# Optimization experiments

Measured on AMD Instinct MI355X. Metric: run time of the kernel, lower is better.

## Reference

```python
import jax, jax.numpy as jnp
import numpy as np

N_INPUT = 2
N_NODES = 4
C = 64          # channel width of every state
B, H, W = 64, 32, 32
N_EDGES = sum(N_INPUT + i for i in range(N_NODES))  # 2+3+4+5 = 14


def conv1x1(x, w):
    # x: [B,C,H,W], w: [C_out,C_in] -> [B,C_out,H,W]
    return jnp.einsum('bchw,oc->bohw', x, w)


def setup_inputs() -> dict:
    key = jax.random.key(0)
    k0, k1, k2, k3 = jax.random.split(key, 4)
    x0 = jax.random.normal(k0, (B, C, H, W), dtype=jnp.float32)
    x1 = jax.random.normal(k1, (B, C, H, W), dtype=jnp.float32)
    # preproc: one 1x1 conv per input state
    W_pre = jax.random.normal(k2, (N_INPUT, C, C), dtype=jnp.float32) * (1.0 / np.sqrt(C))
    # one 1x1 conv per DAG edge (flattened in enumeration order)
    W_edge = jax.random.normal(k3, (N_EDGES, C, C), dtype=jnp.float32) * (1.0 / np.sqrt(C))
    return {'x0': x0, 'x1': x1, 'W_pre': W_pre, 'W_edge': W_edge}


def reference(x0, x1, W_pre, W_edge):
    # preprocess inputs -> initial states
    states = [conv1x1(x0, W_pre[0]), conv1x1(x1, W_pre[1])]
    e = 0
    for i in range(N_NODES):
        n_states = N_INPUT + i
        # gather every prior state, apply edge op (ReLU -> 1x1 conv), sum-merge
        s_cur = conv1x1(jax.nn.relu(states[0]), W_edge[e])
        for s in range(1, n_states):
            s_cur = s_cur + conv1x1(jax.nn.relu(states[s]), W_edge[e + s])
        e += n_states
        states.append(s_cur)
    # merger_out: concat intermediate node states (start=n_input) on channels
    return jnp.concatenate(states[N_INPUT:], axis=1)  # [B, N_NODES*C, H, W]
```

## Files before the change

kernel.cpp:

```cpp
#include <hip/hip_runtime.h>


typedef _Float16 f16;
typedef _Float16 f16x8 __attribute__((ext_vector_type(8)));
typedef float    f32x4 __attribute__((ext_vector_type(4)));

#define RSH 72
#define SB  (64 * RSH)

__device__ __forceinline__ unsigned int pkrtz(float a, float b) {
    __fp16 h2 __attribute__((ext_vector_type(2))) = __builtin_amdgcn_cvt_pkrtz(a, b);
    return __builtin_bit_cast(unsigned int, h2);
}

__global__ __launch_bounds__(256, 2) void dag_kernel(
    const float* __restrict__ x0, const float* __restrict__ x1,
    const float* __restrict__ Wpre, const float* __restrict__ Wedge,
    float* __restrict__ out)
{
    __shared__ __align__(16) f16 lds[7 * SB];

    const int t    = threadIdx.x;
    const int lane = t & 63;
    const int w    = t >> 6;
    const int pl   = lane & 15;
    const int q    = lane >> 4;
    const int mb0  = (w & 1) * 2;
    const int nb0  = (w >> 1) * 2;

    const int blk = blockIdx.x;
    const int b   = blk >> 4;
    const int hw0 = (blk & 15) * 64;

    const float* xg[2] = { x0 + b * 65536 + hw0, x1 + b * 65536 + hw0 };
    float* outg = out + b * 262144 + hw0;

    {
        const int p  = t & 63;
        const int cg = t >> 6;
        #pragma unroll
        for (int inp = 0; inp < 2; ++inp) {
            const float* src = xg[inp] + (cg * 16) * 1024 + p;
            unsigned int u[8];
            #pragma unroll
            for (int i = 0; i < 8; ++i)
                u[i] = pkrtz(src[(2 * i) * 1024], src[(2 * i + 1) * 1024]);
            f16* dst = lds + (3 + inp) * SB + p * RSH + cg * 16;
            ((uint4*)dst)[0] = make_uint4(u[0], u[1], u[2], u[3]);
            ((uint4*)dst)[1] = make_uint4(u[4], u[5], u[6], u[7]);
        }
    }
    {
        const int o = t >> 2, cq = t & 3;
        const float4* ws = (const float4*)(Wpre + o * 64 + cq * 16);
        unsigned int u[8];
        #pragma unroll
        for (int i = 0; i < 4; ++i) {
            float4 v = ws[i];
            u[2 * i]     = pkrtz(v.x, v.y);
            u[2 * i + 1] = pkrtz(v.z, v.w);
        }
        f16* dst = lds + 5 * SB + o * RSH + cq * 16;
        ((uint4*)dst)[0] = make_uint4(u[0], u[1], u[2], u[3]);
        ((uint4*)dst)[1] = make_uint4(u[4], u[5], u[6], u[7]);
    }

    f32x4 acc[2][2] = {};

    #pragma unroll
    for (int k = 0; k < 16; ++k) {
        const int src_tab[16] = { 3,4, 0,1, 0,1,2, 0,1,2,3, 0,1,2,3,4 };
        const int dst_tab[16] = { 0,1, -1,2, -1,-1,3, -1,-1,-1,4, -1,-1,-1,-1,-1 };
        const int out_tab[16] = { -1,-1, -1,0, -1,-1,1, -1,-1,-1,2, -1,-1,-1,-1,3 };

        __syncthreads();

        float4 wr[4];
        if (k < 15) {
            const float* wsrc = ((k + 1 < 2) ? (Wpre + (k + 1) * 4096)
                                             : (Wedge + (k - 1) * 4096))
                                + (t >> 2) * 64 + (t & 3) * 16;
            #pragma unroll
            for (int i = 0; i < 4; ++i) wr[i] = ((const float4*)wsrc)[i];
        }

        const f16* Wl = lds + (5 + (k & 1)) * SB;
        const f16* S  = lds + src_tab[k] * SB;
        #pragma unroll
        for (int kb = 0; kb < 2; ++kb) {
            f16x8 af[2], bf[2];
            #pragma unroll
            for (int i = 0; i < 2; ++i)
                af[i] = *(const f16x8*)(Wl + ((mb0 + i) * 16 + pl) * RSH + kb * 32 + q * 8);
            #pragma unroll
            for (int j = 0; j < 2; ++j)
                bf[j] = *(const f16x8*)(S + ((nb0 + j) * 16 + pl) * RSH + kb * 32 + q * 8);
            #pragma unroll
            for (int i = 0; i < 2; ++i)
                #pragma unroll
                for (int j = 0; j < 2; ++j)
                    acc[i][j] = __builtin_amdgcn_mfma_f32_16x16x32_f16(
                                    af[i], bf[j], acc[i][j], 0, 0, 0);
        }

        if (out_tab[k] >= 0) {
            #pragma unroll
            for (int i = 0; i < 2; ++i)
                #pragma unroll
                for (int j = 0; j < 2; ++j) {
                    const int c = (mb0 + i) * 16 + q * 4;
                    const int p = (nb0 + j) * 16 + pl;
                    #pragma unroll
                    for (int r = 0; r < 4; ++r)
                        outg[(out_tab[k] * 64 + c + r) * 1024 + p] = acc[i][j][r];
                }
        }
        if (dst_tab[k] >= 0) {
            f16* D = lds + dst_tab[k] * SB;
            #pragma unroll
            for (int i = 0; i < 2; ++i)
                #pragma unroll
                for (int j = 0; j < 2; ++j) {
                    const int c = (mb0 + i) * 16 + q * 4;
                    const int p = (nb0 + j) * 16 + pl;
                    unsigned int u0 = pkrtz(fmaxf(acc[i][j][0], 0.f), fmaxf(acc[i][j][1], 0.f));
                    unsigned int u1 = pkrtz(fmaxf(acc[i][j][2], 0.f), fmaxf(acc[i][j][3], 0.f));
                    *(uint2*)(D + p * RSH + c) = make_uint2(u0, u1);
                }
            #pragma unroll
            for (int i = 0; i < 2; ++i)
                #pragma unroll
                for (int j = 0; j < 2; ++j)
                    acc[i][j] = (f32x4){0.f, 0.f, 0.f, 0.f};
        }

        if (k < 15) {
            unsigned int u[8];
            #pragma unroll
            for (int i = 0; i < 4; ++i) {
                u[2 * i]     = pkrtz(wr[i].x, wr[i].y);
                u[2 * i + 1] = pkrtz(wr[i].z, wr[i].w);
            }
            f16* dst = lds + (5 + ((k + 1) & 1)) * SB + (t >> 2) * RSH + (t & 3) * 16;
            ((uint4*)dst)[0] = make_uint4(u[0], u[1], u[2], u[3]);
            ((uint4*)dst)[1] = make_uint4(u[4], u[5], u[6], u[7]);
        }
    }
}

extern "C" void kernel_launch(void* const* d_in, const int* in_sizes, int n_in,
                              void* d_out, int out_size, void* d_ws, size_t ws_size,
                              hipStream_t stream) {
    const float* x0    = (const float*)d_in[0];
    const float* x1    = (const float*)d_in[1];
    const float* Wpre  = (const float*)d_in[2];
    const float* Wedge = (const float*)d_in[3];
    float* outp        = (float*)d_out;
    dag_kernel<<<dim3(1024), dim3(256), 0, stream>>>(x0, x1, Wpre, Wedge, outp);
}
```

Baseline: 114.7 us.

## Pre-convert weights to fp16 MFMA fragments, load into registers, drop per-step barriers

A small pre-kernel converts all 16 weight matrices to fp16 in the MFMA A-fragment layout, stored in the workspace. The main kernel loads each weight matrix straight from global memory into registers, double-buffered one step ahead, instead of staging it through LDS. Each wave now owns a 16-pixel column strip and covers all 64 output channels, so intermediate states are written and read only by the same wave. That removes the per-step __syncthreads, shrinks LDS from 7 to 5 buffers, and raises the occupancy hint to 3 blocks. The costs are an extra kernel launch, more register pressure from holding weight fragments, and redundant global or L2 weight reads in every block.

```diff
diff --git a/kernel.cpp b/kernel.cpp
--- a/kernel.cpp
+++ b/kernel.cpp
@@ -13,20 +13,34 @@
     return __builtin_bit_cast(unsigned int, h2);
 }
 
-__global__ __launch_bounds__(256, 2) void dag_kernel(
+__global__ __launch_bounds__(256) void wconv_kernel(
+    const float* __restrict__ Wpre, const float* __restrict__ Wedge,
+    f16* __restrict__ ws)
+{
+    const int u   = blockIdx.x * 256 + threadIdx.x;
+    const int k   = u >> 9;
+    const int rem = u & 511;
+    const int g   = rem >> 6;
+    const int row = rem & 63;
+    const float* src = ((k < 2) ? (Wpre + k * 4096) : (Wedge + (k - 2) * 4096))
+                       + row * 64 + (g >> 2) * 32 + (g & 3) * 8;
+    float4 v0 = ((const float4*)src)[0];
+    float4 v1 = ((const float4*)src)[1];
+    ((uint4*)ws)[u] = make_uint4(pkrtz(v0.x, v0.y), pkrtz(v0.z, v0.w),
+                                 pkrtz(v1.x, v1.y), pkrtz(v1.z, v1.w));
+}
+
+__global__ __launch_bounds__(256, 3) void dag_kernel(
     const float* __restrict__ x0, const float* __restrict__ x1,
-    const float* __restrict__ Wpre, const float* __restrict__ Wedge,
-    float* __restrict__ out)
+    const f16* __restrict__ wf, float* __restrict__ out)
 {
-    __shared__ __align__(16) f16 lds[7 * SB];
+    __shared__ __align__(16) f16 lds[5 * SB];
 
     const int t    = threadIdx.x;
     const int lane = t & 63;
-    const int w    = t >> 6;
+    const int wv   = t >> 6;
     const int pl   = lane & 15;
     const int q    = lane >> 4;
-    const int mb0  = (w & 1) * 2;
-    const int nb0  = (w >> 1) * 2;
 
     const int blk = blockIdx.x;
     const int b   = blk >> 4;
@@ -35,9 +49,17 @@
     const float* xg[2] = { x0 + b * 65536 + hw0, x1 + b * 65536 + hw0 };
     float* outg = out + b * 262144 + hw0;
 
+    const f16* wl = wf + q * 512 + pl * 8;
+
+    f16x8 wA[2][2][4];
+    #pragma unroll
+    for (int kb = 0; kb < 2; ++kb)
+        #pragma unroll
+        for (int i = 0; i < 4; ++i)
+            wA[0][kb][i] = *(const f16x8*)(wl + kb * 2048 + i * 128);
+
     {
-        const int p  = t & 63;
-        const int cg = t >> 6;
+        const int p = t & 63, cg = t >> 6;
         #pragma unroll
         for (int inp = 0; inp < 2; ++inp) {
             const float* src = xg[inp] + (cg * 16) * 1024 + p;
@@ -50,100 +72,59 @@
             ((uint4*)dst)[1] = make_uint4(u[4], u[5], u[6], u[7]);
         }
     }
-    {
-        const int o = t >> 2, cq = t & 3;
-        const float4* ws = (const float4*)(Wpre + o * 64 + cq * 16);
-        unsigned int u[8];
-        #pragma unroll
-        for (int i = 0; i < 4; ++i) {
-            float4 v = ws[i];
-            u[2 * i]     = pkrtz(v.x, v.y);
-            u[2 * i + 1] = pkrtz(v.z, v.w);
-        }
-        f16* dst = lds + 5 * SB + o * RSH + cq * 16;
-        ((uint4*)dst)[0] = make_uint4(u[0], u[1], u[2], u[3]);
-        ((uint4*)dst)[1] = make_uint4(u[4], u[5], u[6], u[7]);
-    }
+    __syncthreads();
 
-    f32x4 acc[2][2] = {};
+    f32x4 acc[4] = {};
 
     #pragma unroll
     for (int k = 0; k < 16; ++k) {
         const int src_tab[16] = { 3,4, 0,1, 0,1,2, 0,1,2,3, 0,1,2,3,4 };
         const int dst_tab[16] = { 0,1, -1,2, -1,-1,3, -1,-1,-1,4, -1,-1,-1,-1,-1 };
         const int out_tab[16] = { -1,-1, -1,0, -1,-1,1, -1,-1,-1,2, -1,-1,-1,-1,3 };
+        const int cur = k & 1, nxt = cur ^ 1;
 
-        __syncthreads();
-
-        float4 wr[4];
         if (k < 15) {
-            const float* wsrc = ((k + 1 < 2) ? (Wpre + (k + 1) * 4096)
-                                             : (Wedge + (k - 1) * 4096))
-                                + (t >> 2) * 64 + (t & 3) * 16;
+            const f16* wn = wl + (k + 1) * 4096;
             #pragma unroll
-            for (int i = 0; i < 4; ++i) wr[i] = ((const float4*)wsrc)[i];
+            for (int kb = 0; kb < 2; ++kb)
+                #pragma unroll
+                for (int i = 0; i < 4; ++i)
+                    wA[nxt][kb][i] = *(const f16x8*)(wn + kb * 2048 + i * 128);
         }
 
-        const f16* Wl = lds + (5 + (k & 1)) * SB;
-        const f16* S  = lds + src_tab[k] * SB;
+        const f16* S = lds + src_tab[k] * SB + (wv * 16 + pl) * RSH;
+        f16x8 bf[2];
         #pragma unroll
-        for (int kb = 0; kb < 2; ++kb) {
-            f16x8 af[2], bf[2];
+        for (int kb = 0; kb < 2; ++kb)
+            bf[kb] = *(const f16x8*)(S + kb * 32 + q * 8);
+
+        #pragma unroll
+        for (int kb = 0; kb < 2; ++kb)
             #pragma unroll
-            for (int i = 0; i < 2; ++i)
-                af[i] = *(const f16x8*)(Wl + ((mb0 + i) * 16 + pl) * RSH + kb * 32 + q * 8);
-            #pragma unroll
-            for (int j = 0; j < 2; ++j)
-                bf[j] = *(const f16x8*)(S + ((nb0 + j) * 16 + pl) * RSH + kb * 32 + q * 8);
-            #pragma unroll
-            for (int i = 0; i < 2; ++i)
-                #pragma unroll
-                for (int j = 0; j < 2; ++j)
-                    acc[i][j] = __builtin_amdgcn_mfma_f32_16x16x32_f16(
-                                    af[i], bf[j], acc[i][j], 0, 0, 0);
-        }
+            for (int i = 0; i < 4; ++i)
+                acc[i] = __builtin_amdgcn_mfma_f32_16x16x32_f16(
+                             wA[cur][kb][i], bf[kb], acc[i], 0, 0, 0);
 
         if (out_tab[k] >= 0) {
+            const int p = wv * 16 + pl;
             #pragma unroll
-            for (int i = 0; i < 2; ++i)
+            for (int i = 0; i < 4; ++i) {
+                const int c = i * 16 + q * 4;
                 #pragma unroll
-                for (int j = 0; j < 2; ++j) {
-                    const int c = (mb0 + i) * 16 + q * 4;
-                    const int p = (nb0 + j) * 16 + pl;
-                    #pragma unroll
-                    for (int r = 0; r < 4; ++r)
-                        outg[(out_tab[k] * 64 + c + r) * 1024 + p] = acc[i][j][r];
-                }
+                for (int r = 0; r < 4; ++r)
+                    outg[(out_tab[k] * 64 + c + r) * 1024 + p] = acc[i][r];
+            }
         }
         if (dst_tab[k] >= 0) {
-            f16* D = lds + dst_tab[k] * SB;
-            #pragma unroll
-            for (int i = 0; i < 2; ++i)
-                #pragma unroll
-                for (int j = 0; j < 2; ++j) {
-                    const int c = (mb0 + i) * 16 + q * 4;
-                    const int p = (nb0 + j) * 16 + pl;
-                    unsigned int u0 = pkrtz(fmaxf(acc[i][j][0], 0.f), fmaxf(acc[i][j][1], 0.f));
-                    unsigned int u1 = pkrtz(fmaxf(acc[i][j][2], 0.f), fmaxf(acc[i][j][3], 0.f));
-                    *(uint2*)(D + p * RSH + c) = make_uint2(u0, u1);
-                }
-            #pragma unroll
-            for (int i = 0; i < 2; ++i)
-                #pragma unroll
-                for (int j = 0; j < 2; ++j)
-                    acc[i][j] = (f32x4){0.f, 0.f, 0.f, 0.f};
-        }
-
-        if (k < 15) {
-            unsigned int u[8];
+            f16* D = lds + dst_tab[k] * SB + (wv * 16 + pl) * RSH;
             #pragma unroll
             for (int i = 0; i < 4; ++i) {
-                u[2 * i]     = pkrtz(wr[i].x, wr[i].y);
-                u[2 * i + 1] = pkrtz(wr[i].z, wr[i].w);
+                unsigned int u0 = pkrtz(fmaxf(acc[i][0], 0.f), fmaxf(acc[i][1], 0.f));
+                unsigned int u1 = pkrtz(fmaxf(acc[i][2], 0.f), fmaxf(acc[i][3], 0.f));
+                *(uint2*)(D + i * 16 + q * 4) = make_uint2(u0, u1);
             }
-            f16* dst = lds + (5 + ((k + 1) & 1)) * SB + (t >> 2) * RSH + (t & 3) * 16;
-            ((uint4*)dst)[0] = make_uint4(u[0], u[1], u[2], u[3]);
-            ((uint4*)dst)[1] = make_uint4(u[4], u[5], u[6], u[7]);
+            #pragma unroll
+            for (int i = 0; i < 4; ++i) acc[i] = (f32x4){0.f, 0.f, 0.f, 0.f};
         }
     }
 }
@@ -156,5 +137,8 @@
     const float* Wpre  = (const float*)d_in[2];
     const float* Wedge = (const float*)d_in[3];
     float* outp        = (float*)d_out;
-    dag_kernel<<<dim3(1024), dim3(256), 0, stream>>>(x0, x1, Wpre, Wedge, outp);
+    f16*   wfrag       = (f16*)d_ws;
+
+    wconv_kernel<<<dim3(32), dim3(256), 0, stream>>>(Wpre, Wedge, wfrag);
+    dag_kernel<<<dim3(1024), dim3(256), 0, stream>>>(x0, x1, wfrag, outp);
 }
```

New measurement: 109.6 us. 4.4% less time.
